# Kernel optimization log

Measured on AMD Instinct MI355X. Metric: run time of the kernel, lower is better.

## Reference

```python
import jax, jax.numpy as jnp
import numpy as np

BIAS = 1.0
SIGMA = 0.5
EPS = 1e-5


def _mrf_loss(gen, tar):
    # gen, tar: [N, C, H, W]
    N, C, H, W = tar.shape
    meanT = jnp.mean(tar, axis=1, keepdims=True)
    g = gen - meanT
    t = tar - meanT
    g = g / jnp.linalg.norm(g, ord=2, axis=1, keepdims=True)
    t = t / jnp.linalg.norm(t, ord=2, axis=1, keepdims=True)
    # 1x1-patch conv2d with target patches as filters == per-pixel cosine
    # correlation matrix: [N, P=H*W (target positions), H, W (gen positions)]
    tp = t.reshape(N, C, H * W)
    cd = jnp.einsum('nchw,ncp->nphw', g, tp)
    cd = -(cd - 1.0) / 2.0  # cosine distance in [0, 1]
    div = jnp.min(cd, axis=1, keepdims=True)
    rel = cd / (div + EPS)
    e = jnp.exp((BIAS - rel) / SIGMA)
    cs = e / jnp.sum(e, axis=1, keepdims=True)  # sum-normalize over P
    k_max_nc = jnp.max(cs.reshape(N, H * W, -1), axis=2)  # max over gen HW
    div_mrf = jnp.mean(k_max_nc, axis=1)
    return jnp.sum(-jnp.log(div_mrf))


def setup_inputs() -> dict:
    key = jax.random.key(0)
    k1, k2, k3, k4 = jax.random.split(key, 4)
    return {
        'gen3': jax.random.normal(k1, (4, 256, 56, 56), dtype=jnp.float32),
        'tar3': jax.random.normal(k2, (4, 256, 56, 56), dtype=jnp.float32),
        'gen4': jax.random.normal(k3, (4, 512, 28, 28), dtype=jnp.float32),
        'tar4': jax.random.normal(k4, (4, 512, 28, 28), dtype=jnp.float32),
    }


def reference(gen3, tar3, gen4, tar4):
    # weights = [0, 0, 0.5, 1, 0] over VGG relu1..relu5 features
    return 0.5 * _mrf_loss(gen3, tar3) + 1.0 * _mrf_loss(gen4, tar4)
```

## Files before the change

### kernel.cpp

```cpp
#include <hip/hip_runtime.h>
#include <math.h>

typedef __bf16 bf16x8 __attribute__((ext_vector_type(8)));
typedef float f32x4 __attribute__((ext_vector_type(4)));

#define EPSV 1e-5f
#define GLB(p) ((__attribute__((address_space(1))) void*)(p))
#define LDS(p) ((__attribute__((address_space(3))) void*)(p))

__device__ __forceinline__ unsigned fkey(float f) {
  unsigned b = __float_as_uint(f);
  return (b & 0x80000000u) ? ~b : (b | 0x80000000u);
}
__device__ __forceinline__ float funkey(unsigned k) {
  return __uint_as_float((k & 0x80000000u) ? (k & 0x7fffffffu) : ~k);
}

__global__ __launch_bounds__(256) void norm_kernel(
    const float* __restrict__ g3, const float* __restrict__ t3,
    __bf16* __restrict__ G3, __bf16* __restrict__ T3,
    const float* __restrict__ g4, const float* __restrict__ t4,
    __bf16* __restrict__ G4, __bf16* __restrict__ T4)
{
  int lay = blockIdx.z >> 2, n = blockIdx.z & 3;
  const float *gen, *tar; __bf16 *Gh, *Th; int C, P, Ppad, PT, NWORK, NTOT, NG;
  if (lay == 0) { gen = g3; tar = t3; Gh = G3; Th = T3; C = 256; P = 3136; Ppad = 3200; PT = 32; NWORK = 98; NTOT = 100; NG = 8; }
  else          { gen = g4; tar = t4; Gh = G4; Th = T4; C = 512; P = 784;  Ppad = 896;  PT = 16; NWORK = 49; NTOT = 56;  NG = 16; }
  if (blockIdx.y >= (unsigned)NTOT) return;
  int pl, cg;
  if (lay == 0) { pl = threadIdx.x & 31; cg = threadIdx.x >> 5; }
  else          { pl = threadIdx.x & 15; cg = threadIdx.x >> 4; }
  int c0 = cg * 32;

  if (blockIdx.y >= (unsigned)NWORK) {
    int p = P + (blockIdx.y - NWORK) * PT + pl;
    if (p < Ppad) {
      __bf16* tp = Th + ((size_t)n * Ppad + p) * C + c0;
      __bf16* gp = Gh + ((size_t)n * Ppad + p) * C + c0;
      bf16x8 z;
      for (int j = 0; j < 8; j++) z[j] = (__bf16)0.f;
      for (int j = 0; j < 32; j += 8) { *(bf16x8*)(tp + j) = z; *(bf16x8*)(gp + j) = z; }
    }
    return;
  }

  int p = blockIdx.y * PT + pl;
  const float* tb = tar + (size_t)n * C * P + (size_t)c0 * P + p;
  const float* gb = gen + (size_t)n * C * P + (size_t)c0 * P + p;
  float tv[32], gv[32];
  float st = 0.f, sst = 0.f, sg = 0.f, ssg = 0.f;
#pragma unroll
  for (int j = 0; j < 32; j++) {
    tv[j] = tb[(size_t)j * P];
    gv[j] = gb[(size_t)j * P];
  }
#pragma unroll
  for (int j = 0; j < 32; j++) {
    st += tv[j]; sst += tv[j] * tv[j];
    sg += gv[j]; ssg += gv[j] * gv[j];
  }
  __shared__ f32x4 red[16][32];
  red[cg][pl] = f32x4{st, sst, sg, ssg};
  __syncthreads();
  for (int h = NG >> 1; h > 0; h >>= 1) {
    if (cg < h) {
      f32x4 a = red[cg][pl], b = red[cg + h][pl];
      red[cg][pl] = f32x4{a[0] + b[0], a[1] + b[1], a[2] + b[2], a[3] + b[3]};
    }
    __syncthreads();
  }
  f32x4 s = red[0][pl];
  float m = s[0] / (float)C;
  float vt = s[1] - s[0] * s[0] / (float)C;
  float vg = s[3] - 2.f * m * s[2] + (float)C * m * m;
  float it = rsqrtf(fmaxf(vt, 1e-30f));
  float ig = rsqrtf(fmaxf(vg, 1e-30f));
  __bf16* tp = Th + ((size_t)n * Ppad + p) * C + c0;
  __bf16* gp = Gh + ((size_t)n * Ppad + p) * C + c0;
#pragma unroll
  for (int j0 = 0; j0 < 32; j0 += 8) {
    bf16x8 to, go;
    for (int j = 0; j < 8; j++) {
      to[j] = (__bf16)((tv[j0 + j] - m) * it);
      go[j] = (__bf16)((gv[j0 + j] - m) * ig);
    }
    *(bf16x8*)(tp + j0) = to;
    *(bf16x8*)(gp + j0) = go;
  }
}

__global__ __launch_bounds__(256, 3) void gemm_kernel(
    const __bf16* __restrict__ A3, const __bf16* __restrict__ B3,
    __bf16* __restrict__ So3, unsigned* __restrict__ dk3,
    const __bf16* __restrict__ A4, const __bf16* __restrict__ B4,
    __bf16* __restrict__ So4, unsigned* __restrict__ dk4)
{
  __shared__ __attribute__((aligned(16))) char smem[37888];

  int id = blockIdx.x;
  const __bf16 *A, *B; __bf16* S; unsigned* dk;
  int C, Ppad, Qpad, Preal, NT, n, t;
  if (id < 2500) {
    n = id / 625; t = id - n * 625;
    A = A3; B = B3; S = So3; dk = dk3; C = 256; Ppad = 3200; Qpad = 3200; Preal = 3136; NT = 25;
  } else {
    id -= 2500;
    n = id / 49; t = id - n * 49;
    A = A4; B = B4; S = So4; dk = dk4; C = 512; Ppad = 896;  Qpad = 896;  Preal = 784;  NT = 7;
  }
  int bpb = NT * 8;
  int b = t / bpb, r = t - b * bpb;
  int rem = NT - b * 8;
  int h = rem < 8 ? rem : 8;
  int pt = b * 8 + r % h, qt = r / h;
  int p0 = pt * 128, q0 = qt * 128;

  int tid = threadIdx.x;
  int w = tid >> 6, lane = tid & 63;
  int lm = lane & 15, lq = lane >> 4;
  int wrow = (w >> 1) * 64, wcol = (w & 1) * 64;

  int srow = tid >> 2;
  int scol = ((tid & 3) ^ ((tid >> 3) & 3)) * 8;
  const __bf16* gA = A + ((size_t)n * Ppad + p0 + srow) * C + scol;
  const __bf16* gB = B + ((size_t)n * Qpad + q0 + srow) * C + scol;
  size_t rowoff = (size_t)64 * C;

  int sl = lq ^ ((lm >> 1) & 3);
  int aoff = (wrow + lm) * 64 + sl * 16;
  int boff = (wcol + lm) * 64 + sl * 16;

  f32x4 acc[4][4];
  for (int i = 0; i < 4; i++)
    for (int j = 0; j < 4; j++)
      acc[i][j] = f32x4{0.f, 0.f, 0.f, 0.f};

  for (int k0 = 0; k0 < C; k0 += 64) {
    __syncthreads();
#pragma unroll
    for (int sub = 0; sub < 2; sub++) {
      int kk = k0 + sub * 32;
      char* a = smem + sub * 8192 + w * 1024;
      char* bb = smem + 16384 + sub * 8192 + w * 1024;
      __builtin_amdgcn_global_load_lds(GLB(gA + kk), LDS(a), 16, 0, 0);
      __builtin_amdgcn_global_load_lds(GLB(gA + rowoff + kk), LDS(a + 4096), 16, 0, 0);
      __builtin_amdgcn_global_load_lds(GLB(gB + kk), LDS(bb), 16, 0, 0);
      __builtin_amdgcn_global_load_lds(GLB(gB + rowoff + kk), LDS(bb + 4096), 16, 0, 0);
    }
    __syncthreads();
#pragma unroll
    for (int sub = 0; sub < 2; sub++) {
      const char* ab = smem + sub * 8192;
      const char* bb = smem + 16384 + sub * 8192;
      bf16x8 af[4], bf[4];
      for (int i = 0; i < 4; i++) af[i] = *(const bf16x8*)(ab + aoff + i * 1024);
      for (int j = 0; j < 4; j++) bf[j] = *(const bf16x8*)(bb + boff + j * 1024);
      for (int i = 0; i < 4; i++)
        for (int j = 0; j < 4; j++)
          acc[i][j] = __builtin_amdgcn_mfma_f32_16x16x32_bf16(af[i], bf[j], acc[i][j], 0, 0, 0);
    }
  }

  float cm[4] = {-INFINITY, -INFINITY, -INFINITY, -INFINITY};
  for (int i = 0; i < 4; i++)
    for (int j = 0; j < 4; j++)
      for (int ri = 0; ri < 4; ri++) {
        int pr = p0 + wrow + i * 16 + lq * 4 + ri;
        if (pr < Preal) cm[j] = fmaxf(cm[j], (float)(__bf16)acc[i][j][ri]);
      }

  __syncthreads();
  for (int i = 0; i < 4; i++) {
    for (int j = 0; j < 4; j++) {
      int row = wrow + i * 16 + lq * 4;
      int col = wcol + j * 16 + lm;
      for (int ri = 0; ri < 4; ri++)
        *(__bf16*)(smem + (row + ri) * 296 + col * 2) = (__bf16)acc[i][j][ri];
    }
  }
  __syncthreads();
  __bf16* Sb = S + (size_t)n * Ppad * Qpad;
  int rr = tid >> 4, cc8 = (tid & 15) * 8;
  for (int r8 = 0; r8 < 8; r8++) {
    int row = r8 * 16 + rr;
    bf16x8 v = *(const bf16x8*)(smem + row * 296 + cc8 * 2);
    __builtin_nontemporal_store(v, (bf16x8*)(Sb + (size_t)(p0 + row) * Qpad + q0 + cc8));
  }

  for (int j = 0; j < 4; j++) {
    float v = cm[j];
    v = fmaxf(v, __shfl_xor(v, 16, 64));
    v = fmaxf(v, __shfl_xor(v, 32, 64));
    if (lq == 0 && v > -INFINITY) {
      int qc = q0 + wcol + j * 16 + lm;
      atomicMax(&dk[(size_t)n * Qpad + qc], fkey(v));
    }
  }
}

__global__ __launch_bounds__(256) void z_kernel(
    const __bf16* __restrict__ S3, const unsigned* __restrict__ dk3, float* __restrict__ Zp3,
    const __bf16* __restrict__ S4, const unsigned* __restrict__ dk4, float* __restrict__ Zp4)
{
  int id = blockIdx.x;
  const __bf16* S; const unsigned* dk; float* Zp;
  int Ppad, Qreal, Qpad, NSL, SLAB, n, qx, sy;
  if (id < 784) {
    n = id / 196; int r = id - n * 196; sy = r >> 1; qx = r & 1;
    S = S3; dk = dk3; Zp = Zp3; Ppad = 3200; Qreal = 3136; Qpad = 3200; NSL = 98; SLAB = 32;
  } else {
    id -= 784;
    n = id / 49; sy = id - n * 49; qx = 0;
    S = S4; dk = dk4; Zp = Zp4; Ppad = 896;  Qreal = 784;  Qpad = 896;  NSL = 49; SLAB = 16;
  }
  int q = (qx * 256 + threadIdx.x) * 8;
  if (q >= Qreal) return;
  float idv[8], nid[8];
  const unsigned* dkp = dk + (size_t)n * Qpad + q;
#pragma unroll
  for (int j = 0; j < 8; j++) {
    float mx = funkey(dkp[j]);
    float d = 0.5f * (1.f - mx) + EPSV;
    idv[j] = 1.f / d;
    nid[j] = -idv[j];
  }
  int p0 = sy * SLAB;
  const __bf16* Sp = S + (size_t)n * Ppad * Qpad + q;
  float acc[8] = {0.f, 0.f, 0.f, 0.f, 0.f, 0.f, 0.f, 0.f};
  for (int pb = 0; pb < SLAB; pb += 8) {
    bf16x8 sv[8];
#pragma unroll
    for (int r = 0; r < 8; r++)
      sv[r] = *(const bf16x8*)(Sp + (size_t)(p0 + pb + r) * Qpad);
#pragma unroll
    for (int r = 0; r < 8; r++)
      for (int j = 0; j < 8; j++)
        acc[j] += __expf(fmaf((float)sv[r][j], idv[j], nid[j]));
  }
  float* zp = Zp + ((size_t)n * NSL + sy) * Qpad + q;
  *(f32x4*)zp = f32x4{acc[0], acc[1], acc[2], acc[3]};
  *(f32x4*)(zp + 4) = f32x4{acc[4], acc[5], acc[6], acc[7]};
}

__global__ __launch_bounds__(256) void reduce_kernel(
    const float* __restrict__ Zp3, const unsigned* __restrict__ dk3,
    float* __restrict__ invd3, float* __restrict__ c3,
    const float* __restrict__ Zp4, const unsigned* __restrict__ dk4,
    float* __restrict__ invd4, float* __restrict__ c4)
{
  int lay = blockIdx.y >> 2, n = blockIdx.y & 3;
  const float* Zp; const unsigned* dk; float *invd, *c; int Qreal, Qpad, NSL;
  if (lay == 0) { Zp = Zp3; dk = dk3; invd = invd3; c = c3; Qreal = 3136; Qpad = 3200; NSL = 98; }
  else          { Zp = Zp4; dk = dk4; invd = invd4; c = c4; Qreal = 784;  Qpad = 896;  NSL = 49; }
  int q = blockIdx.x * 256 + threadIdx.x;
  if (q >= Qreal) return;
  float s0 = 0.f, s1 = 0.f, s2 = 0.f, s3 = 0.f;
  int sl = 0;
  for (; sl + 4 <= NSL; sl += 4) {
    s0 += Zp[((size_t)n * NSL + sl) * Qpad + q];
    s1 += Zp[((size_t)n * NSL + sl + 1) * Qpad + q];
    s2 += Zp[((size_t)n * NSL + sl + 2) * Qpad + q];
    s3 += Zp[((size_t)n * NSL + sl + 3) * Qpad + q];
  }
  for (; sl < NSL; sl++) s0 += Zp[((size_t)n * NSL + sl) * Qpad + q];
  float s = (s0 + s1) + (s2 + s3);
  float mx = funkey(dk[(size_t)n * Qpad + q]);
  float d = 0.5f * (1.f - mx) + EPSV;
  float idv = 1.f / d;
  invd[(size_t)n * Qpad + q] = idv;
  c[(size_t)n * Qpad + q] = -logf(s) - idv;
}

__global__ __launch_bounds__(256) void rowmax_kernel(
    const __bf16* __restrict__ S3, const float* __restrict__ invd3,
    const float* __restrict__ c3, float* __restrict__ km3,
    const __bf16* __restrict__ S4, const float* __restrict__ invd4,
    const float* __restrict__ c4, float* __restrict__ km4)
{
  int id = blockIdx.x;
  const __bf16* S; const float *invd, *cc; float* kmax;
  int Qreal, Qpad, Ppad, n, blk;
  if (id < 1568) {
    n = id / 392; blk = id - n * 392;
    S = S3; invd = invd3; cc = c3; kmax = km3; Qreal = 3136; Qpad = 3200; Ppad = 3200;
  } else {
    id -= 1568;
    n = id / 98; blk = id - n * 98;
    S = S4; invd = invd4; cc = c4; kmax = km4; Qreal = 784;  Qpad = 896;  Ppad = 896;
  }
  int p0 = blk * 8;
  const __bf16* Sp = S + ((size_t)n * Ppad + p0) * Qpad;
  const float* idp = invd + (size_t)n * Qpad;
  const float* cp = cc + (size_t)n * Qpad;
  int nq8 = Qreal >> 3;
  float m[8];
#pragma unroll
  for (int r = 0; r < 8; r++) m[r] = -INFINITY;
  for (int i = threadIdx.x; i < nq8; i += 256) {
    f32x4 i0 = *(const f32x4*)(idp + (size_t)i * 8);
    f32x4 i1 = *(const f32x4*)(idp + (size_t)i * 8 + 4);
    f32x4 c0 = *(const f32x4*)(cp + (size_t)i * 8);
    f32x4 c1 = *(const f32x4*)(cp + (size_t)i * 8 + 4);
#pragma unroll
    for (int r = 0; r < 8; r++) {
      bf16x8 sv = *(const bf16x8*)(Sp + (size_t)r * Qpad + (size_t)i * 8);
      for (int j = 0; j < 4; j++)
        m[r] = fmaxf(m[r], fmaf((float)sv[j], i0[j], c0[j]));
      for (int j = 0; j < 4; j++)
        m[r] = fmaxf(m[r], fmaf((float)sv[j + 4], i1[j], c1[j]));
    }
  }
#pragma unroll
  for (int r = 0; r < 8; r++)
    for (int off = 32; off > 0; off >>= 1)
      m[r] = fmaxf(m[r], __shfl_xor(m[r], off, 64));
  __shared__ float red[4][8];
  int w = threadIdx.x >> 6;
  if ((threadIdx.x & 63) == 0)
    for (int r = 0; r < 8; r++) red[w][r] = m[r];
  __syncthreads();
  if (threadIdx.x < 8) {
    int r = threadIdx.x;
    float mr = fmaxf(fmaxf(red[0][r], red[1][r]), fmaxf(red[2][r], red[3][r]));
    kmax[(size_t)n * Ppad + p0 + r] = __expf(mr);
  }
}

__global__ void final_kernel(const float* __restrict__ kmax3, const float* __restrict__ kmax4,
                             float* __restrict__ out)
{
  __shared__ float red[256];
  int tid = threadIdx.x;
  float total = 0.f;
  for (int l = 0; l < 2; l++) {
    const float* km = l ? kmax4 : kmax3;
    int P = l ? 784 : 3136;
    int Ppad = l ? 896 : 3200;
    float wgt = l ? 1.0f : 0.5f;
    for (int n = 0; n < 4; n++) {
      float s = 0.f;
      for (int i = tid; i < P; i += 256) s += km[(size_t)n * Ppad + i];
      red[tid] = s;
      __syncthreads();
      for (int st = 128; st > 0; st >>= 1) {
        if (tid < st) red[tid] += red[tid + st];
        __syncthreads();
      }
      if (tid == 0) total += wgt * (-logf(red[0] / (float)P));
      __syncthreads();
    }
  }
  if (tid == 0) out[0] = total;
}

extern "C" void kernel_launch(void* const* d_in, const int* in_sizes, int n_in,
                              void* d_out, int out_size, void* d_ws, size_t ws_size,
                              hipStream_t stream)
{
  const float* gen3 = (const float*)d_in[0];
  const float* tar3 = (const float*)d_in[1];
  const float* gen4 = (const float*)d_in[2];
  const float* tar4 = (const float*)d_in[3];

  char* ws = (char*)d_ws;
  size_t off = 0;
  auto take = [&](size_t bytes) { char* p = ws + off; off += bytes; return p; };

  unsigned* divkey3 = (unsigned*)take(51200);
  unsigned* divkey4 = (unsigned*)take(14336);
  size_t zero_bytes = off;
  __bf16* That3 = (__bf16*)take(6553600);
  __bf16* Ghat3 = (__bf16*)take(6553600);
  __bf16* That4 = (__bf16*)take(3670016);
  __bf16* Ghat4 = (__bf16*)take(3670016);
  __bf16* S3    = (__bf16*)take(81920000);
  __bf16* S4    = (__bf16*)take(6422528);
  float*  Zp3   = (float*) take(5017600);
  float*  Zp4   = (float*) take(702464);
  float* invd3  = (float*)take(51200);
  float* c3     = (float*)take(51200);
  float* kmax3  = (float*)take(51200);
  float* invd4  = (float*)take(14336);
  float* c4     = (float*)take(14336);
  float* kmax4  = (float*)take(14336);

  hipMemsetAsync(divkey3, 0, zero_bytes, stream);

  norm_kernel<<<dim3(1, 100, 8), 256, 0, stream>>>(gen3, tar3, Ghat3, That3,
                                                   gen4, tar4, Ghat4, That4);
  gemm_kernel<<<2696, 256, 0, stream>>>(That3, Ghat3, S3, divkey3,
                                        That4, Ghat4, S4, divkey4);
  z_kernel<<<980, 256, 0, stream>>>(S3, divkey3, Zp3,
                                    S4, divkey4, Zp4);
  reduce_kernel<<<dim3(13, 8), 256, 0, stream>>>(Zp3, divkey3, invd3, c3,
                                                 Zp4, divkey4, invd4, c4);
  rowmax_kernel<<<1960, 256, 0, stream>>>(S3, invd3, c3, kmax3,
                                          S4, invd4, c4, kmax4);
  final_kernel<<<1, 256, 0, stream>>>(kmax3, kmax4, (float*)d_out);
}
```

Before: 204.9 us.

## Load GEMM fragments directly from global memory with register double-buffering

The GEMM kernel stops staging A/B tiles through LDS with global_load_lds and barriers. Each lane now reads its MFMA fragments straight from global memory into registers, using a two-stage register double buffer so the next k-slice loads while the current one feeds the MFMAs. This removes the per-k-step __syncthreads and LDS traffic, but each tile is now re-read by several waves through the cache, and the 16-byte row-strided loads are less coalesced. Separately, the exp-sum kernel now loads 16 rows per batch instead of 8, giving more memory-level parallelism at the cost of more registers.

```diff
diff --git a/kernel.cpp b/kernel.cpp
--- a/kernel.cpp
+++ b/kernel.cpp
@@ -5,8 +5,6 @@
 typedef float f32x4 __attribute__((ext_vector_type(4)));
 
 #define EPSV 1e-5f
-#define GLB(p) ((__attribute__((address_space(1))) void*)(p))
-#define LDS(p) ((__attribute__((address_space(3))) void*)(p))
 
 __device__ __forceinline__ unsigned fkey(float f) {
   unsigned b = __float_as_uint(f);
@@ -120,46 +118,40 @@
   int lm = lane & 15, lq = lane >> 4;
   int wrow = (w >> 1) * 64, wcol = (w & 1) * 64;
 
-  int srow = tid >> 2;
-  int scol = ((tid & 3) ^ ((tid >> 3) & 3)) * 8;
-  const __bf16* gA = A + ((size_t)n * Ppad + p0 + srow) * C + scol;
-  const __bf16* gB = B + ((size_t)n * Qpad + q0 + srow) * C + scol;
-  size_t rowoff = (size_t)64 * C;
-
-  int sl = lq ^ ((lm >> 1) & 3);
-  int aoff = (wrow + lm) * 64 + sl * 16;
-  int boff = (wcol + lm) * 64 + sl * 16;
+  const __bf16* aBase = A + ((size_t)n * Ppad + p0 + wrow + lm) * C + lq * 8;
+  const __bf16* bBase = B + ((size_t)n * Qpad + q0 + wcol + lm) * C + lq * 8;
+  size_t rstep = (size_t)16 * C;
 
   f32x4 acc[4][4];
   for (int i = 0; i < 4; i++)
     for (int j = 0; j < 4; j++)
       acc[i][j] = f32x4{0.f, 0.f, 0.f, 0.f};
 
-  for (int k0 = 0; k0 < C; k0 += 64) {
-    __syncthreads();
-#pragma unroll
-    for (int sub = 0; sub < 2; sub++) {
-      int kk = k0 + sub * 32;
-      char* a = smem + sub * 8192 + w * 1024;
-      char* bb = smem + 16384 + sub * 8192 + w * 1024;
-      __builtin_amdgcn_global_load_lds(GLB(gA + kk), LDS(a), 16, 0, 0);
-      __builtin_amdgcn_global_load_lds(GLB(gA + rowoff + kk), LDS(a + 4096), 16, 0, 0);
-      __builtin_amdgcn_global_load_lds(GLB(gB + kk), LDS(bb), 16, 0, 0);
-      __builtin_amdgcn_global_load_lds(GLB(gB + rowoff + kk), LDS(bb + 4096), 16, 0, 0);
-    }
-    __syncthreads();
-#pragma unroll
-    for (int sub = 0; sub < 2; sub++) {
-      const char* ab = smem + sub * 8192;
-      const char* bb = smem + 16384 + sub * 8192;
-      bf16x8 af[4], bf[4];
-      for (int i = 0; i < 4; i++) af[i] = *(const bf16x8*)(ab + aoff + i * 1024);
-      for (int j = 0; j < 4; j++) bf[j] = *(const bf16x8*)(bb + boff + j * 1024);
-      for (int i = 0; i < 4; i++)
-        for (int j = 0; j < 4; j++)
-          acc[i][j] = __builtin_amdgcn_mfma_f32_16x16x32_bf16(af[i], bf[j], acc[i][j], 0, 0, 0);
-    }
-  }
+  bf16x8 a0[4], b0[4], a1[4], b1[4];
+  auto loadf = [&](int k, bf16x8* af, bf16x8* bf) {
+#pragma unroll
+    for (int i = 0; i < 4; i++) af[i] = *(const bf16x8*)(aBase + (size_t)i * rstep + k);
+#pragma unroll
+    for (int j = 0; j < 4; j++) bf[j] = *(const bf16x8*)(bBase + (size_t)j * rstep + k);
+  };
+  auto domfma = [&](bf16x8* af, bf16x8* bf) {
+#pragma unroll
+    for (int i = 0; i < 4; i++)
+#pragma unroll
+      for (int j = 0; j < 4; j++)
+        acc[i][j] = __builtin_amdgcn_mfma_f32_16x16x32_bf16(af[i], bf[j], acc[i][j], 0, 0, 0);
+  };
+
+  int nk = C >> 5;
+  loadf(0, a0, b0);
+  int k = 32;
+  for (int it = 0; it < (nk >> 1) - 1; it++) {
+    loadf(k, a1, b1); domfma(a0, b0); k += 32;
+    loadf(k, a0, b0); domfma(a1, b1); k += 32;
+  }
+  loadf(k, a1, b1);
+  domfma(a0, b0);
+  domfma(a1, b1);
 
   float cm[4] = {-INFINITY, -INFINITY, -INFINITY, -INFINITY};
   for (int i = 0; i < 4; i++)
@@ -169,7 +161,6 @@
         if (pr < Preal) cm[j] = fmaxf(cm[j], (float)(__bf16)acc[i][j][ri]);
       }
 
-  __syncthreads();
   for (int i = 0; i < 4; i++) {
     for (int j = 0; j < 4; j++) {
       int row = wrow + i * 16 + lq * 4;
@@ -227,13 +218,13 @@
   int p0 = sy * SLAB;
   const __bf16* Sp = S + (size_t)n * Ppad * Qpad + q;
   float acc[8] = {0.f, 0.f, 0.f, 0.f, 0.f, 0.f, 0.f, 0.f};
-  for (int pb = 0; pb < SLAB; pb += 8) {
-    bf16x8 sv[8];
-#pragma unroll
-    for (int r = 0; r < 8; r++)
+  for (int pb = 0; pb < SLAB; pb += 16) {
+    bf16x8 sv[16];
+#pragma unroll
+    for (int r = 0; r < 16; r++)
       sv[r] = *(const bf16x8*)(Sp + (size_t)(p0 + pb + r) * Qpad);
 #pragma unroll
-    for (int r = 0; r < 8; r++)
+    for (int r = 0; r < 16; r++)
       for (int j = 0; j < 8; j++)
         acc[j] += __expf(fmaf((float)sv[r][j], idv[j], nid[j]));
   }
```

Measured after the change: 258.9 us. 1.26x slower.

## Replace atomic column-max with per-tile partial buffer and separate reduction kernel

Applied to the files above, without the earlier changes.

The GEMM kernel no longer does global atomicMax on sign-flipped keys to find each column's maximum correlation. Each row-half of a tile now writes its partial column max to a dedicated buffer, and a new invd_kernel reduces those partials and computes the inverse divisor once. That removes the memset and the atomics, and z/reduce reuse the precomputed inverse. Occupancy hint for the GEMM is raised from 3 to 4 blocks per CU, which may force register spills, and an extra small kernel launch is added.

```diff
diff --git a/kernel.cpp b/kernel.cpp
--- a/kernel.cpp
+++ b/kernel.cpp
@@ -7,14 +7,6 @@
 #define EPSV 1e-5f
 #define GLB(p) ((__attribute__((address_space(1))) void*)(p))
 #define LDS(p) ((__attribute__((address_space(3))) void*)(p))
-
-__device__ __forceinline__ unsigned fkey(float f) {
-  unsigned b = __float_as_uint(f);
-  return (b & 0x80000000u) ? ~b : (b | 0x80000000u);
-}
-__device__ __forceinline__ float funkey(unsigned k) {
-  return __uint_as_float((k & 0x80000000u) ? (k & 0x7fffffffu) : ~k);
-}
 
 __global__ __launch_bounds__(256) void norm_kernel(
     const float* __restrict__ g3, const float* __restrict__ t3,
@@ -89,24 +81,24 @@
   }
 }
 
-__global__ __launch_bounds__(256, 3) void gemm_kernel(
+__global__ __launch_bounds__(256, 4) void gemm_kernel(
     const __bf16* __restrict__ A3, const __bf16* __restrict__ B3,
-    __bf16* __restrict__ So3, unsigned* __restrict__ dk3,
+    __bf16* __restrict__ So3, float* __restrict__ Cm3,
     const __bf16* __restrict__ A4, const __bf16* __restrict__ B4,
-    __bf16* __restrict__ So4, unsigned* __restrict__ dk4)
+    __bf16* __restrict__ So4, float* __restrict__ Cm4)
 {
   __shared__ __attribute__((aligned(16))) char smem[37888];
 
   int id = blockIdx.x;
-  const __bf16 *A, *B; __bf16* S; unsigned* dk;
+  const __bf16 *A, *B; __bf16* S; float* Cm;
   int C, Ppad, Qpad, Preal, NT, n, t;
   if (id < 2500) {
     n = id / 625; t = id - n * 625;
-    A = A3; B = B3; S = So3; dk = dk3; C = 256; Ppad = 3200; Qpad = 3200; Preal = 3136; NT = 25;
+    A = A3; B = B3; S = So3; Cm = Cm3; C = 256; Ppad = 3200; Qpad = 3200; Preal = 3136; NT = 25;
   } else {
     id -= 2500;
     n = id / 49; t = id - n * 49;
-    A = A4; B = B4; S = So4; dk = dk4; C = 512; Ppad = 896;  Qpad = 896;  Preal = 784;  NT = 7;
+    A = A4; B = B4; S = So4; Cm = Cm4; C = 512; Ppad = 896;  Qpad = 896;  Preal = 784;  NT = 7;
   }
   int bpb = NT * 8;
   int b = t / bpb, r = t - b * bpb;
@@ -191,37 +183,52 @@
     float v = cm[j];
     v = fmaxf(v, __shfl_xor(v, 16, 64));
     v = fmaxf(v, __shfl_xor(v, 32, 64));
-    if (lq == 0 && v > -INFINITY) {
+    if (lq == 0) {
       int qc = q0 + wcol + j * 16 + lm;
-      atomicMax(&dk[(size_t)n * Qpad + qc], fkey(v));
-    }
-  }
+      Cm[((size_t)n * NT * 2 + pt * 2 + (w >> 1)) * Qpad + qc] = v;
+    }
+  }
+}
+
+__global__ __launch_bounds__(256) void invd_kernel(
+    const float* __restrict__ Cm3, float* __restrict__ invd3,
+    const float* __restrict__ Cm4, float* __restrict__ invd4)
+{
+  int lay = blockIdx.y >> 2, n = blockIdx.y & 3;
+  const float* Cm; float* invd; int Qreal, Qpad, NP;
+  if (lay == 0) { Cm = Cm3; invd = invd3; Qreal = 3136; Qpad = 3200; NP = 50; }
+  else          { Cm = Cm4; invd = invd4; Qreal = 784;  Qpad = 896;  NP = 14; }
+  int q = blockIdx.x * 256 + threadIdx.x;
+  if (q >= Qreal) return;
+  float mx = -INFINITY;
+  for (int i = 0; i < NP; i++)
+    mx = fmaxf(mx, Cm[((size_t)n * NP + i) * Qpad + q]);
+  float d = 0.5f * (1.f - mx) + EPSV;
+  invd[(size_t)n * Qpad + q] = 1.f / d;
 }
 
 __global__ __launch_bounds__(256) void z_kernel(
-    const __bf16* __restrict__ S3, const unsigned* __restrict__ dk3, float* __restrict__ Zp3,
-    const __bf16* __restrict__ S4, const unsigned* __restrict__ dk4, float* __restrict__ Zp4)
+    const __bf16* __restrict__ S3, const float* __restrict__ invd3, float* __restrict__ Zp3,
+    const __bf16* __restrict__ S4, const float* __restrict__ invd4, float* __restrict__ Zp4)
 {
   int id = blockIdx.x;
-  const __bf16* S; const unsigned* dk; float* Zp;
+  const __bf16* S; const float* invd; float* Zp;
   int Ppad, Qreal, Qpad, NSL, SLAB, n, qx, sy;
   if (id < 784) {
     n = id / 196; int r = id - n * 196; sy = r >> 1; qx = r & 1;
-    S = S3; dk = dk3; Zp = Zp3; Ppad = 3200; Qreal = 3136; Qpad = 3200; NSL = 98; SLAB = 32;
+    S = S3; invd = invd3; Zp = Zp3; Ppad = 3200; Qreal = 3136; Qpad = 3200; NSL = 98; SLAB = 32;
   } else {
     id -= 784;
     n = id / 49; sy = id - n * 49; qx = 0;
-    S = S4; dk = dk4; Zp = Zp4; Ppad = 896;  Qreal = 784;  Qpad = 896;  NSL = 49; SLAB = 16;
+    S = S4; invd = invd4; Zp = Zp4; Ppad = 896;  Qreal = 784;  Qpad = 896;  NSL = 49; SLAB = 16;
   }
   int q = (qx * 256 + threadIdx.x) * 8;
   if (q >= Qreal) return;
   float idv[8], nid[8];
-  const unsigned* dkp = dk + (size_t)n * Qpad + q;
+  const float* ip = invd + (size_t)n * Qpad + q;
 #pragma unroll
   for (int j = 0; j < 8; j++) {
-    float mx = funkey(dkp[j]);
-    float d = 0.5f * (1.f - mx) + EPSV;
-    idv[j] = 1.f / d;
+    idv[j] = ip[j];
     nid[j] = -idv[j];
   }
   int p0 = sy * SLAB;
@@ -243,15 +250,13 @@
 }
 
 __global__ __launch_bounds__(256) void reduce_kernel(
-    const float* __restrict__ Zp3, const unsigned* __restrict__ dk3,
-    float* __restrict__ invd3, float* __restrict__ c3,
-    const float* __restrict__ Zp4, const unsigned* __restrict__ dk4,
-    float* __restrict__ invd4, float* __restrict__ c4)
+    const float* __restrict__ Zp3, const float* __restrict__ invd3, float* __restrict__ c3,
+    const float* __restrict__ Zp4, const float* __restrict__ invd4, float* __restrict__ c4)
 {
   int lay = blockIdx.y >> 2, n = blockIdx.y & 3;
-  const float* Zp; const unsigned* dk; float *invd, *c; int Qreal, Qpad, NSL;
-  if (lay == 0) { Zp = Zp3; dk = dk3; invd = invd3; c = c3; Qreal = 3136; Qpad = 3200; NSL = 98; }
-  else          { Zp = Zp4; dk = dk4; invd = invd4; c = c4; Qreal = 784;  Qpad = 896;  NSL = 49; }
+  const float *Zp, *invd; float* c; int Qreal, Qpad, NSL;
+  if (lay == 0) { Zp = Zp3; invd = invd3; c = c3; Qreal = 3136; Qpad = 3200; NSL = 98; }
+  else          { Zp = Zp4; invd = invd4; c = c4; Qreal = 784;  Qpad = 896;  NSL = 49; }
   int q = blockIdx.x * 256 + threadIdx.x;
   if (q >= Qreal) return;
   float s0 = 0.f, s1 = 0.f, s2 = 0.f, s3 = 0.f;
@@ -264,11 +269,7 @@
   }
   for (; sl < NSL; sl++) s0 += Zp[((size_t)n * NSL + sl) * Qpad + q];
   float s = (s0 + s1) + (s2 + s3);
-  float mx = funkey(dk[(size_t)n * Qpad + q]);
-  float d = 0.5f * (1.f - mx) + EPSV;
-  float idv = 1.f / d;
-  invd[(size_t)n * Qpad + q] = idv;
-  c[(size_t)n * Qpad + q] = -logf(s) - idv;
+  c[(size_t)n * Qpad + q] = -logf(s) - invd[(size_t)n * Qpad + q];
 }
 
 __global__ __launch_bounds__(256) void rowmax_kernel(
@@ -366,15 +367,14 @@
   size_t off = 0;
   auto take = [&](size_t bytes) { char* p = ws + off; off += bytes; return p; };
 
-  unsigned* divkey3 = (unsigned*)take(51200);
-  unsigned* divkey4 = (unsigned*)take(14336);
-  size_t zero_bytes = off;
   __bf16* That3 = (__bf16*)take(6553600);
   __bf16* Ghat3 = (__bf16*)take(6553600);
   __bf16* That4 = (__bf16*)take(3670016);
   __bf16* Ghat4 = (__bf16*)take(3670016);
   __bf16* S3    = (__bf16*)take(81920000);
   __bf16* S4    = (__bf16*)take(6422528);
+  float*  Cm3   = (float*) take(2560000);
+  float*  Cm4   = (float*) take(200704);
   float*  Zp3   = (float*) take(5017600);
   float*  Zp4   = (float*) take(702464);
   float* invd3  = (float*)take(51200);
@@ -384,16 +384,15 @@
   float* c4     = (float*)take(14336);
   float* kmax4  = (float*)take(14336);
 
-  hipMemsetAsync(divkey3, 0, zero_bytes, stream);
-
   norm_kernel<<<dim3(1, 100, 8), 256, 0, stream>>>(gen3, tar3, Ghat3, That3,
                                                    gen4, tar4, Ghat4, That4);
-  gemm_kernel<<<2696, 256, 0, stream>>>(That3, Ghat3, S3, divkey3,
-                                        That4, Ghat4, S4, divkey4);
-  z_kernel<<<980, 256, 0, stream>>>(S3, divkey3, Zp3,
-                                    S4, divkey4, Zp4);
-  reduce_kernel<<<dim3(13, 8), 256, 0, stream>>>(Zp3, divkey3, invd3, c3,
-                                                 Zp4, divkey4, invd4, c4);
+  gemm_kernel<<<2696, 256, 0, stream>>>(That3, Ghat3, S3, Cm3,
+                                        That4, Ghat4, S4, Cm4);
+  invd_kernel<<<dim3(13, 8), 256, 0, stream>>>(Cm3, invd3, Cm4, invd4);
+  z_kernel<<<980, 256, 0, stream>>>(S3, invd3, Zp3,
+                                    S4, invd4, Zp4);
+  reduce_kernel<<<dim3(13, 8), 256, 0, stream>>>(Zp3, invd3, c3,
+                                                 Zp4, invd4, c4);
   rowmax_kernel<<<1960, 256, 0, stream>>>(S3, invd3, c3, kmax3,
                                           S4, invd4, c4, kmax4);
   final_kernel<<<1, 256, 0, stream>>>(kmax3, kmax4, (float*)d_out);
```

Measured after the change: 209.6 us. 2.3% more time.
